# Performance work log

Hardware: AMD Instinct MI355X
Metric: run time of the kernel (lower is better)

Reference implementation:

```python
import jax, jax.numpy as jnp
import numpy as np

D_MODEL = 1024
NUM_HEADS = 16
HEAD_DIM = D_MODEL // NUM_HEADS
SEQ_LEN = 2048
BATCH = 2
THETA = 10000.0


def apply_rope(x, token_positions):
    # x: (..., seq, head_dim); token_positions: (seq,)
    d_k = x.shape[-1]
    inv_freq = 1.0 / (THETA ** (jnp.arange(0, d_k, 2, dtype=jnp.float32) / d_k))  # (d_k/2,)
    angle = token_positions.astype(jnp.float32)[:, None] * inv_freq[None, :]       # (seq, d_k/2)
    cos, sin = jnp.cos(angle), jnp.sin(angle)
    xr = x.reshape(*x.shape[:-1], d_k // 2, 2)
    a, b = xr[..., 0], xr[..., 1]  # real, imag parts of consecutive pairs
    # complex multiply (a + ib) * (cos + i sin)
    out_r = a * cos - b * sin
    out_i = a * sin + b * cos
    return jnp.stack([out_r, out_i], axis=-1).reshape(x.shape)


def setup_inputs() -> dict:
    key = jax.random.key(0)
    ks = jax.random.split(key, 5)
    std = np.sqrt(2.0 / (D_MODEL + D_MODEL))
    return {
        "x": jax.random.normal(ks[0], (BATCH, SEQ_LEN, D_MODEL), dtype=jnp.float32),
        "Wq": jax.random.normal(ks[1], (D_MODEL, D_MODEL), dtype=jnp.float32) * std,
        "Wk": jax.random.normal(ks[2], (D_MODEL, D_MODEL), dtype=jnp.float32) * std,
        "Wv": jax.random.normal(ks[3], (D_MODEL, D_MODEL), dtype=jnp.float32) * std,
        "Wo": jax.random.normal(ks[4], (D_MODEL, D_MODEL), dtype=jnp.float32) * std,
        "token_positions": jnp.arange(SEQ_LEN, dtype=jnp.int32),
    }


def reference(x, Wq, Wk, Wv, Wo, token_positions):
    B, L, D = x.shape
    H, Dh = NUM_HEADS, HEAD_DIM

    def proj(W):  # '... d_in, d_out d_in -> ... d_out' then split heads -> (B,H,L,Dh)
        y = jnp.einsum('bld,ed->ble', x, W)
        return y.reshape(B, L, H, Dh).transpose(0, 2, 1, 3)

    q = apply_rope(proj(Wq), token_positions)
    k = apply_rope(proj(Wk), token_positions)
    v = proj(Wv)

    scores = jnp.einsum('bhqd,bhkd->bhqk', q, k) / jnp.sqrt(jnp.float32(Dh))  # (B,H,L,L)
    causal = jnp.tril(jnp.ones((L, L), dtype=bool))
    scores = jnp.where(causal, scores, -jnp.inf)
    attn = jax.nn.softmax(scores, axis=-1)
    o = jnp.einsum('bhqk,bhkd->bhqd', attn, v)  # (B,H,L,Dh)
    o = o.transpose(0, 2, 1, 3).reshape(B, L, D)
    return jnp.einsum('bld,ed->ble', o, Wo)
```

## Files before the change

kernel.cpp:

```cpp
#include <hip/hip_runtime.h>

typedef __bf16 bf16;
typedef __attribute__((ext_vector_type(8))) __bf16 bf16x8;
typedef __attribute__((ext_vector_type(4))) __bf16 bf16x4;
typedef __attribute__((ext_vector_type(4))) float f32x4;

__device__ inline bf16 f2bf(float f) {
  unsigned u = __builtin_bit_cast(unsigned, f);
  u += 0x7fff + ((u >> 16) & 1);
  unsigned short h = (unsigned short)(u >> 16);
  return __builtin_bit_cast(bf16, h);
}

__device__ inline void gl_lds16(const bf16* g, bf16* l) {
  __builtin_amdgcn_global_load_lds(
      (const __attribute__((address_space(1))) void*)g,
      (__attribute__((address_space(3))) void*)l, 16, 0, 0);
}

__global__ __launch_bounds__(256) void cvt_kernel(
    const float* __restrict__ x, const float* __restrict__ wq,
    const float* __restrict__ wk, const float* __restrict__ wv,
    const float* __restrict__ wo, bf16* __restrict__ dst,
    const int* __restrict__ pos, float* __restrict__ tab) {
  if (blockIdx.x >= 8192) {
    int gid = (blockIdx.x - 8192) * 256 + threadIdx.x;
    int tok = gid >> 5, j = gid & 31;
    float freq = exp2f(-(float)(2 * j) * 0.20762051f);
    float angle = (float)pos[tok] * freq;
    float sn, cs;
    sincosf(angle, &sn, &cs);
    *(float2*)(tab + tok * 64 + j * 2) = make_float2(cs, sn);
    return;
  }
  int idx = (blockIdx.x * 256 + threadIdx.x) * 4;
  const float* src;
  if (idx < 4194304) {
    src = x + idx;
  } else {
    int j = idx - 4194304;
    int w = j >> 20;
    const float* sw = (w == 0) ? wq : (w == 1) ? wk : (w == 2) ? wv : wo;
    src = sw + (j & 1048575);
  }
  float4 f = *(const float4*)src;
  bf16x4 o = {f2bf(f.x), f2bf(f.y), f2bf(f.z), f2bf(f.w)};
  *(bf16x4*)(dst + idx) = o;
}

__global__ __launch_bounds__(256) void gemm_qkv_kernel(
    const bf16* __restrict__ xb, const bf16* __restrict__ wb,
    const float* __restrict__ tab,
    bf16* __restrict__ Qb, bf16* __restrict__ Kb, bf16* __restrict__ Vtb) {
  __shared__ __align__(16) bf16 smem[16384];
  int tid = threadIdx.x;
  int lane = tid & 63, w = tid >> 6;
  int l15 = lane & 15, quad = lane >> 4;
  int bid = blockIdx.x;
  int xcd = bid & 7, j = bid >> 3;
  int by = (xcd & 3) * 8 + (j & 7);
  int bx = (xcd >> 2) * 12 + (j >> 3);
  int mb = by * 128, nb = bx * 128;
  int mq = (w & 1) * 64, nq = (w >> 1) * 64;
  int rq = lane >> 2;
  int gsrc = (lane & 3) ^ (rq & 3) ^ (lane >> 4);
  const bf16* agp0 = xb + (size_t)(mb + w * 32 + rq) * 1024 + gsrc * 8;
  const bf16* agp1 = agp0 + 16 * 1024;
  const bf16* bgp0 = wb + (size_t)(nb + w * 32 + rq) * 1024 + gsrc * 8;
  const bf16* bgp1 = bgp0 + 16 * 1024;
  f32x4 acc[4][4];
#pragma unroll
  for (int i = 0; i < 4; ++i)
#pragma unroll
    for (int j2 = 0; j2 < 4; ++j2)
      for (int r = 0; r < 4; ++r) acc[i][j2][r] = 0.f;
  gl_lds16(agp0, smem + w * 1024);
  gl_lds16(agp1, smem + w * 1024 + 512);
  gl_lds16(bgp0, smem + 4096 + w * 1024);
  gl_lds16(bgp1, smem + 4096 + w * 1024 + 512);
  agp0 += 32; agp1 += 32; bgp0 += 32; bgp1 += 32;
  __syncthreads();
  int rg = quad ^ (l15 & 3) ^ (l15 >> 2);
  for (int kt = 0; kt < 32; ++kt) {
    bf16* Ab = smem + (kt & 1) * 8192;
    bf16* Bb = Ab + 4096;
    if (kt < 31) {
      bf16* An = smem + ((kt & 1) ^ 1) * 8192;
      bf16* Bn = An + 4096;
      gl_lds16(agp0, An + w * 1024);
      gl_lds16(agp1, An + w * 1024 + 512);
      gl_lds16(bgp0, Bn + w * 1024);
      gl_lds16(bgp1, Bn + w * 1024 + 512);
      agp0 += 32; agp1 += 32; bgp0 += 32; bgp1 += 32;
    }
    bf16x8 af[4], bfr[4];
#pragma unroll
    for (int mt = 0; mt < 4; ++mt)
      af[mt] = *(const bf16x8*)(Ab + (mq + mt * 16 + l15) * 32 + rg * 8);
#pragma unroll
    for (int nt = 0; nt < 4; ++nt)
      bfr[nt] = *(const bf16x8*)(Bb + (nq + nt * 16 + l15) * 32 + rg * 8);
#pragma unroll
    for (int mt = 0; mt < 4; ++mt)
#pragma unroll
      for (int nt = 0; nt < 4; ++nt)
        acc[mt][nt] = __builtin_amdgcn_mfma_f32_16x16x32_bf16(af[mt], bfr[nt], acc[mt][nt], 0, 0, 0);
    __syncthreads();
  }
  int b = mb >> 11;
  int mtok = mb & 2047;
  if (bx < 16) {
    bf16* dst = (bx < 8) ? Qb : Kb;
#pragma unroll
    for (int nt = 0; nt < 4; ++nt) {
      int e = nb + nq + nt * 16 + l15;
      int d = e & 63;
      int h = (e & 1023) >> 6;
      int tbase = d & ~1;
#pragma unroll
      for (int mt = 0; mt < 4; ++mt) {
#pragma unroll
        for (int r = 0; r < 4; ++r) {
          int ltok = mtok + mq + mt * 16 + quad * 4 + r;
          float val = acc[mt][nt][r];
          float p = __shfl_xor(val, 1);
          float2 cs2 = *(const float2*)(tab + ltok * 64 + tbase);
          float outv = (e & 1) ? (p * cs2.y + val * cs2.x) : (val * cs2.x - p * cs2.y);
          dst[(size_t)(((b << 4) + h) * 2048 + ltok) * 64 + d] = f2bf(outv);
        }
      }
    }
  } else {
    bf16* T = smem;
    for (int h2 = 0; h2 < 2; ++h2) {
      if ((w >> 1) == h2) {
#pragma unroll
        for (int nt = 0; nt < 4; ++nt)
#pragma unroll
          for (int mt = 0; mt < 4; ++mt) {
            bf16x4 tv = {f2bf(acc[mt][nt][0]), f2bf(acc[mt][nt][1]),
                         f2bf(acc[mt][nt][2]), f2bf(acc[mt][nt][3])};
            *(bf16x4*)&T[(nt * 16 + l15) * 136 + mq + mt * 16 + quad * 4] = tv;
          }
      }
      __syncthreads();
      int row = tid >> 2, cs = (tid & 3) * 32;
      int e = nb + h2 * 64 + row;
      int d = e & 63, hh = (e & 1023) >> 6;
      bf16* vdst = Vtb + ((size_t)((b << 4) + hh) * 64 + d) * 2048 + mtok + cs;
#pragma unroll
      for (int j3 = 0; j3 < 4; ++j3)
        *(bf16x8*)(vdst + j3 * 8) = *(const bf16x8*)&T[row * 136 + cs + j3 * 8];
      __syncthreads();
    }
  }
}

#define SCALE_L2E 0.18033688f
__global__ __launch_bounds__(256) void attn_kernel(
    const bf16* __restrict__ Qb, const bf16* __restrict__ Kb,
    const bf16* __restrict__ Vtb, bf16* __restrict__ Ob) {
  __shared__ __align__(16) bf16 Ks[64 * 64];
  __shared__ __align__(16) bf16 Vs[64 * 64];
  __shared__ __align__(16) bf16 pbuf[4][16 * 72];
  int tid = threadIdx.x;
  int lane = tid & 63, w = tid >> 6;
  int l15 = lane & 15, quad = lane >> 4;
  int bidx = blockIdx.x;
  int bh = bidx & 31;
  int qt = 31 - (bidx >> 5);
  int qbase = qt * 64;
  const bf16* Qp = Qb + (size_t)bh * 131072;
  const bf16* Kp = Kb + (size_t)bh * 131072;
  const bf16* Vp = Vtb + (size_t)bh * 131072;
  int r8 = lane >> 3;
  int gsw8 = (lane & 7) ^ r8;
  int g0 = quad ^ (l15 & 7);
  int g1 = (4 + quad) ^ (l15 & 7);
  bf16x8 qf[2];
#pragma unroll
  for (int c = 0; c < 2; ++c)
    qf[c] = *(const bf16x8*)(Qp + (size_t)(qbase + w * 16 + l15) * 64 + c * 32 + quad * 8);
  f32x4 oacc[4];
#pragma unroll
  for (int dt = 0; dt < 4; ++dt)
    for (int r = 0; r < 4; ++r) oacc[dt][r] = 0.f;
  float lpart = 0.f;
  int qmin_w = qbase + w * 16;
  int ntiles = qt + 1;

  {
    const bf16* ksrc = Kp + (size_t)(w * 16 + r8) * 64 + gsw8 * 8;
    bf16* kdst = &Ks[(w * 16) * 64];
    gl_lds16(ksrc, kdst);
    gl_lds16(ksrc + 8 * 64, kdst + 8 * 64);
    const bf16* vsrc = Vp + (size_t)(w * 16 + r8) * 2048 + gsw8 * 8;
    bf16* vdst = &Vs[(w * 16) * 64];
    gl_lds16(vsrc, vdst);
    gl_lds16(vsrc + 8 * 2048, vdst + 8 * 64);
  }
  __syncthreads();

  for (int t = 0; t < ntiles; ++t) {
    int kb = t * 64;
    bool pf = (t + 1 < ntiles);
    bf16x8 rk0, rk1, rv0, rv1;
    if (pf) {
      const bf16* ksrc = Kp + (size_t)(kb + 64 + w * 16 + r8) * 64 + gsw8 * 8;
      rk0 = *(const bf16x8*)ksrc;
      rk1 = *(const bf16x8*)(ksrc + 8 * 64);
      const bf16* vsrc = Vp + (size_t)(w * 16 + r8) * 2048 + kb + 64 + gsw8 * 8;
      rv0 = *(const bf16x8*)vsrc;
      rv1 = *(const bf16x8*)(vsrc + 8 * 2048);
    }
    {
      bf16x8 kf[4][2], vf[4][2];
#pragma unroll
      for (int kt = 0; kt < 4; ++kt) {
        kf[kt][0] = *(const bf16x8*)(&Ks[(kt * 16 + l15) * 64 + g0 * 8]);
        kf[kt][1] = *(const bf16x8*)(&Ks[(kt * 16 + l15) * 64 + g1 * 8]);
      }
#pragma unroll
      for (int dt = 0; dt < 4; ++dt) {
        vf[dt][0] = *(const bf16x8*)(&Vs[(dt * 16 + l15) * 64 + g0 * 8]);
        vf[dt][1] = *(const bf16x8*)(&Vs[(dt * 16 + l15) * 64 + g1 * 8]);
      }
      int q = qmin_w + l15;
      f32x4 s[4];
#pragma unroll
      for (int kt = 0; kt < 4; ++kt) {
        for (int r = 0; r < 4; ++r) s[kt][r] = 0.f;
        s[kt] = __builtin_amdgcn_mfma_f32_16x16x32_bf16(kf[kt][0], qf[0], s[kt], 0, 0, 0);
        s[kt] = __builtin_amdgcn_mfma_f32_16x16x32_bf16(kf[kt][1], qf[1], s[kt], 0, 0, 0);
      }
      float pe[16];
      if (kb + 63 > qmin_w) {
#pragma unroll
        for (int kt = 0; kt < 4; ++kt)
#pragma unroll
          for (int r = 0; r < 4; ++r) {
            int key = kb + kt * 16 + quad * 4 + r;
            pe[kt * 4 + r] = (key <= q) ? exp2f(s[kt][r] * SCALE_L2E) : 0.f;
          }
      } else {
#pragma unroll
        for (int kt = 0; kt < 4; ++kt)
#pragma unroll
          for (int r = 0; r < 4; ++r) pe[kt * 4 + r] = exp2f(s[kt][r] * SCALE_L2E);
      }
#pragma unroll
      for (int i = 0; i < 16; ++i) lpart += pe[i];
#pragma unroll
      for (int kt = 0; kt < 4; ++kt) {
        bf16x4 pw = {f2bf(pe[kt * 4]), f2bf(pe[kt * 4 + 1]), f2bf(pe[kt * 4 + 2]), f2bf(pe[kt * 4 + 3])};
        *(bf16x4*)&pbuf[w][l15 * 72 + kt * 16 + quad * 4] = pw;
      }
      bf16x8 pb0 = *(const bf16x8*)&pbuf[w][l15 * 72 + quad * 8];
      bf16x8 pb1 = *(const bf16x8*)&pbuf[w][l15 * 72 + 32 + quad * 8];
#pragma unroll
      for (int dt = 0; dt < 4; ++dt) {
        oacc[dt] = __builtin_amdgcn_mfma_f32_16x16x32_bf16(vf[dt][0], pb0, oacc[dt], 0, 0, 0);
        oacc[dt] = __builtin_amdgcn_mfma_f32_16x16x32_bf16(vf[dt][1], pb1, oacc[dt], 0, 0, 0);
      }
    }
    __syncthreads();
    if (pf) {
      bf16* kd = &Ks[(w * 16) * 64] + lane * 8;
      *(bf16x8*)kd = rk0;
      *(bf16x8*)(kd + 512) = rk1;
      bf16* vd = &Vs[(w * 16) * 64] + lane * 8;
      *(bf16x8*)vd = rv0;
      *(bf16x8*)(vd + 512) = rv1;
    }
    __syncthreads();
  }
  float lrun = lpart;
  lrun += __shfl_xor(lrun, 16);
  lrun += __shfl_xor(lrun, 32);
  int b0 = bh >> 4, h = bh & 15;
  float inv = 1.f / lrun;
  int q = qmin_w + l15;
  bf16* obase = Ob + ((size_t)(b0 * 2048 + q)) * 1024 + h * 64;
#pragma unroll
  for (int dt = 0; dt < 4; ++dt)
#pragma unroll
    for (int r = 0; r < 4; ++r)
      obase[dt * 16 + quad * 4 + r] = f2bf(oacc[dt][r] * inv);
}

__global__ __launch_bounds__(256) void gemm_out_kernel(
    const bf16* __restrict__ Ob, const bf16* __restrict__ wob,
    float* __restrict__ out) {
  __shared__ __align__(16) bf16 As[128 * 64];
  __shared__ __align__(16) bf16 Bs[64 * 64];
  int tid = threadIdx.x;
  int lane = tid & 63, w = tid >> 6;
  int l15 = lane & 15, quad = lane >> 4;
  int bid = blockIdx.x;
  int xcd = bid & 7, j = bid >> 3;
  int by = (xcd & 3) * 8 + (j & 7);
  int bx = (xcd >> 2) * 8 + (j >> 3);
  int mb = by * 128, nb = bx * 64;
  int mq = (w & 1) * 64, nq = (w >> 1) * 32;
  int gsw = (lane & 7) ^ ((lane >> 3) & 7);
  const bf16* agp = Ob + (size_t)(mb + w * 32 + (lane >> 3)) * 1024 + gsw * 8;
  const bf16* bgp = wob + (size_t)(nb + w * 16 + (lane >> 3)) * 1024 + gsw * 8;
  bf16* alp = As + (w * 32) * 64;
  bf16* blp = Bs + (w * 16) * 64;
  f32x4 acc[4][2];
#pragma unroll
  for (int i = 0; i < 4; ++i)
#pragma unroll
    for (int j2 = 0; j2 < 2; ++j2)
      for (int r = 0; r < 4; ++r) acc[i][j2][r] = 0.f;
  for (int kt = 0; kt < 16; ++kt) {
#pragma unroll
    for (int i = 0; i < 4; ++i)
      gl_lds16(agp + i * 8192, alp + i * 512);
#pragma unroll
    for (int i = 0; i < 2; ++i)
      gl_lds16(bgp + i * 8192, blp + i * 512);
    agp += 64; bgp += 64;
    __syncthreads();
#pragma unroll
    for (int c = 0; c < 2; ++c) {
      bf16x8 af[4], bfr[2];
      int rg = (c * 4 + quad);
#pragma unroll
      for (int mt = 0; mt < 4; ++mt)
        af[mt] = *(const bf16x8*)(As + (mq + mt * 16 + l15) * 64 + (rg ^ (l15 & 7)) * 8);
#pragma unroll
      for (int nt = 0; nt < 2; ++nt)
        bfr[nt] = *(const bf16x8*)(Bs + (nq + nt * 16 + l15) * 64 + (rg ^ (l15 & 7)) * 8);
#pragma unroll
      for (int mt = 0; mt < 4; ++mt)
#pragma unroll
        for (int nt = 0; nt < 2; ++nt)
          acc[mt][nt] = __builtin_amdgcn_mfma_f32_16x16x32_bf16(af[mt], bfr[nt], acc[mt][nt], 0, 0, 0);
    }
    __syncthreads();
  }
#pragma unroll
  for (int mt = 0; mt < 4; ++mt)
#pragma unroll
    for (int nt = 0; nt < 2; ++nt)
#pragma unroll
      for (int r = 0; r < 4; ++r)
        out[(size_t)(mb + mq + mt * 16 + quad * 4 + r) * 1024 + nb + nq + nt * 16 + l15] = acc[mt][nt][r];
}

extern "C" void kernel_launch(void* const* d_in, const int* in_sizes, int n_in,
                              void* d_out, int out_size, void* d_ws, size_t ws_size,
                              hipStream_t stream) {
  const float* x  = (const float*)d_in[0];
  const float* wq = (const float*)d_in[1];
  const float* wk = (const float*)d_in[2];
  const float* wv = (const float*)d_in[3];
  const float* wo = (const float*)d_in[4];
  const int* pos  = (const int*)d_in[5];
  float* out = (float*)d_out;
  bf16* wsb = (bf16*)d_ws;
  bf16* xb  = wsb;
  bf16* wb  = wsb + 4194304;
  bf16* Qb  = wsb + 8388608;
  bf16* Kb  = wsb + 12582912;
  bf16* Vtb = wsb + 16777216;
  bf16* Obf = wsb + 20971520;
  float* tab = (float*)Obf;
  hipLaunchKernelGGL(cvt_kernel, dim3(8448), dim3(256), 0, stream, x, wq, wk, wv, wo, wsb, pos, tab);
  hipLaunchKernelGGL(gemm_qkv_kernel, dim3(768), dim3(256), 0, stream, xb, wb, tab, Qb, Kb, Vtb);
  hipLaunchKernelGGL(attn_kernel, dim3(1024), dim3(256), 0, stream, Qb, Kb, Vtb, Obf);
  hipLaunchKernelGGL(gemm_out_kernel, dim3(512), dim3(256), 0, stream, Obf, wb + 3 * 1048576, out);
}
```

Measured before the change: 190.2 us.

## Load QKV A-operand directly to registers; double-buffer output GEMM LDS

In the QKV projection GEMM, the activation operand is no longer staged through LDS. Each wave loads its own A fragments straight from global memory into registers, ping-ponging between two register sets, and only the weight tile stays double-buffered in LDS, which shrinks shared memory. The output projection GEMM moves from a single-buffered 64-wide K tile with a sync before compute to a double-buffered 32-wide K tile that prefetches the next tile while computing. The aim is to cut LDS traffic and footprint and to hide global load latency. The cost is more register pressure and uncoalesced per-lane global reads for the A operand.

```diff
diff --git a/kernel.cpp b/kernel.cpp
--- a/kernel.cpp
+++ b/kernel.cpp
@@ -52,7 +52,7 @@
     const bf16* __restrict__ xb, const bf16* __restrict__ wb,
     const float* __restrict__ tab,
     bf16* __restrict__ Qb, bf16* __restrict__ Kb, bf16* __restrict__ Vtb) {
-  __shared__ __align__(16) bf16 smem[16384];
+  __shared__ __align__(16) bf16 smem[8704];
   int tid = threadIdx.x;
   int lane = tid & 63, w = tid >> 6;
   int l15 = lane & 15, quad = lane >> 4;
@@ -64,49 +64,58 @@
   int mq = (w & 1) * 64, nq = (w >> 1) * 64;
   int rq = lane >> 2;
   int gsrc = (lane & 3) ^ (rq & 3) ^ (lane >> 4);
-  const bf16* agp0 = xb + (size_t)(mb + w * 32 + rq) * 1024 + gsrc * 8;
-  const bf16* agp1 = agp0 + 16 * 1024;
   const bf16* bgp0 = wb + (size_t)(nb + w * 32 + rq) * 1024 + gsrc * 8;
   const bf16* bgp1 = bgp0 + 16 * 1024;
+  const bf16* agp = xb + (size_t)(mb + mq + l15) * 1024 + quad * 8;
   f32x4 acc[4][4];
 #pragma unroll
   for (int i = 0; i < 4; ++i)
 #pragma unroll
     for (int j2 = 0; j2 < 4; ++j2)
       for (int r = 0; r < 4; ++r) acc[i][j2][r] = 0.f;
-  gl_lds16(agp0, smem + w * 1024);
-  gl_lds16(agp1, smem + w * 1024 + 512);
-  gl_lds16(bgp0, smem + 4096 + w * 1024);
-  gl_lds16(bgp1, smem + 4096 + w * 1024 + 512);
-  agp0 += 32; agp1 += 32; bgp0 += 32; bgp1 += 32;
+  bf16x8 afA[4], afB[4];
+  gl_lds16(bgp0, smem + w * 1024);
+  gl_lds16(bgp1, smem + w * 1024 + 512);
+  bgp0 += 32; bgp1 += 32;
+#pragma unroll
+  for (int mt = 0; mt < 4; ++mt)
+    afA[mt] = *(const bf16x8*)(agp + mt * 16384);
   __syncthreads();
   int rg = quad ^ (l15 & 3) ^ (l15 >> 2);
-  for (int kt = 0; kt < 32; ++kt) {
-    bf16* Ab = smem + (kt & 1) * 8192;
-    bf16* Bb = Ab + 4096;
-    if (kt < 31) {
-      bf16* An = smem + ((kt & 1) ^ 1) * 8192;
-      bf16* Bn = An + 4096;
-      gl_lds16(agp0, An + w * 1024);
-      gl_lds16(agp1, An + w * 1024 + 512);
-      gl_lds16(bgp0, Bn + w * 1024);
-      gl_lds16(bgp1, Bn + w * 1024 + 512);
-      agp0 += 32; agp1 += 32; bgp0 += 32; bgp1 += 32;
-    }
-    bf16x8 af[4], bfr[4];
-#pragma unroll
-    for (int mt = 0; mt < 4; ++mt)
-      af[mt] = *(const bf16x8*)(Ab + (mq + mt * 16 + l15) * 32 + rg * 8);
-#pragma unroll
-    for (int nt = 0; nt < 4; ++nt)
-      bfr[nt] = *(const bf16x8*)(Bb + (nq + nt * 16 + l15) * 32 + rg * 8);
-#pragma unroll
-    for (int mt = 0; mt < 4; ++mt)
-#pragma unroll
-      for (int nt = 0; nt < 4; ++nt)
-        acc[mt][nt] = __builtin_amdgcn_mfma_f32_16x16x32_bf16(af[mt], bfr[nt], acc[mt][nt], 0, 0, 0);
-    __syncthreads();
-  }
+
+#define QKV_STEP(AFC, AFN)                                                    \
+  {                                                                           \
+    bf16* Bb = smem + (kt & 1) * 4096;                                        \
+    if (kt < 31) {       \
+      bf16* Bn = smem + ((kt & 1) ^ 1) * 4096;                                \
+      gl_lds16(bgp0, Bn + w * 1024);                                          \
+      gl_lds16(bgp1, Bn + w * 1024 + 512);                                    \
+      bgp0 += 32; bgp1 += 32;                                                 \
+      _Pragma("unroll") for (int mt = 0; mt < 4; ++mt)                        \
+          AFN[mt] = *(const bf16x8*)(agp + 32 + mt * 16384);                  \
+      agp += 32;                                                              \
+    }                                                                         \
+    bf16x8 bfr[4];                                                            \
+    _Pragma("unroll") for (int nt = 0; nt < 4; ++nt)                          \
+        bfr[nt] = *(const bf16x8*)(Bb + (nq + nt * 16 + l15) * 32 + rg * 8);  \
+    _Pragma("unroll") for (int mt = 0; mt < 4; ++mt)                          \
+        _Pragma("unroll") for (int nt = 0; nt < 4; ++nt)                      \
+            acc[mt][nt] = __builtin_amdgcn_mfma_f32_16x16x32_bf16(            \
+                AFC[mt], bfr[nt], acc[mt][nt], 0, 0, 0);                      \
+    __syncthreads();                                                          \
+  }
+
+  int kt = 0;
+  for (;;) {
+    QKV_STEP(afA, afB);
+    ++kt;
+    if (kt >= 32) break;
+    QKV_STEP(afB, afA);
+    ++kt;
+    if (kt >= 32) break;
+  }
+#undef QKV_STEP
+
   int b = mb >> 11;
   int mtok = mb & 2047;
   if (bx < 16) {
@@ -291,8 +300,7 @@
 __global__ __launch_bounds__(256) void gemm_out_kernel(
     const bf16* __restrict__ Ob, const bf16* __restrict__ wob,
     float* __restrict__ out) {
-  __shared__ __align__(16) bf16 As[128 * 64];
-  __shared__ __align__(16) bf16 Bs[64 * 64];
+  __shared__ __align__(16) bf16 smem[12288];
   int tid = threadIdx.x;
   int lane = tid & 63, w = tid >> 6;
   int l15 = lane & 15, quad = lane >> 4;
@@ -302,42 +310,45 @@
   int bx = (xcd >> 2) * 8 + (j >> 3);
   int mb = by * 128, nb = bx * 64;
   int mq = (w & 1) * 64, nq = (w >> 1) * 32;
-  int gsw = (lane & 7) ^ ((lane >> 3) & 7);
-  const bf16* agp = Ob + (size_t)(mb + w * 32 + (lane >> 3)) * 1024 + gsw * 8;
-  const bf16* bgp = wob + (size_t)(nb + w * 16 + (lane >> 3)) * 1024 + gsw * 8;
-  bf16* alp = As + (w * 32) * 64;
-  bf16* blp = Bs + (w * 16) * 64;
+  int rq = lane >> 2;
+  int gsrc = (lane & 3) ^ (rq & 3) ^ (lane >> 4);
+  const bf16* agp0 = Ob + (size_t)(mb + w * 32 + rq) * 1024 + gsrc * 8;
+  const bf16* agp1 = agp0 + 16 * 1024;
+  const bf16* bgp0 = wob + (size_t)(nb + w * 16 + rq) * 1024 + gsrc * 8;
   f32x4 acc[4][2];
 #pragma unroll
   for (int i = 0; i < 4; ++i)
 #pragma unroll
     for (int j2 = 0; j2 < 2; ++j2)
       for (int r = 0; r < 4; ++r) acc[i][j2][r] = 0.f;
-  for (int kt = 0; kt < 16; ++kt) {
-#pragma unroll
-    for (int i = 0; i < 4; ++i)
-      gl_lds16(agp + i * 8192, alp + i * 512);
-#pragma unroll
-    for (int i = 0; i < 2; ++i)
-      gl_lds16(bgp + i * 8192, blp + i * 512);
-    agp += 64; bgp += 64;
-    __syncthreads();
-#pragma unroll
-    for (int c = 0; c < 2; ++c) {
-      bf16x8 af[4], bfr[2];
-      int rg = (c * 4 + quad);
-#pragma unroll
-      for (int mt = 0; mt < 4; ++mt)
-        af[mt] = *(const bf16x8*)(As + (mq + mt * 16 + l15) * 64 + (rg ^ (l15 & 7)) * 8);
+  gl_lds16(agp0, smem + w * 1024);
+  gl_lds16(agp1, smem + w * 1024 + 512);
+  gl_lds16(bgp0, smem + 4096 + w * 512);
+  agp0 += 32; agp1 += 32; bgp0 += 32;
+  __syncthreads();
+  int rg = quad ^ (l15 & 3) ^ (l15 >> 2);
+  for (int kt = 0; kt < 32; ++kt) {
+    bf16* Ab = smem + (kt & 1) * 6144;
+    bf16* Bb = Ab + 4096;
+    if (kt < 31) {
+      bf16* An = smem + ((kt & 1) ^ 1) * 6144;
+      gl_lds16(agp0, An + w * 1024);
+      gl_lds16(agp1, An + w * 1024 + 512);
+      gl_lds16(bgp0, An + 4096 + w * 512);
+      agp0 += 32; agp1 += 32; bgp0 += 32;
+    }
+    bf16x8 af[4], bfr[2];
+#pragma unroll
+    for (int mt = 0; mt < 4; ++mt)
+      af[mt] = *(const bf16x8*)(Ab + (mq + mt * 16 + l15) * 32 + rg * 8);
+#pragma unroll
+    for (int nt = 0; nt < 2; ++nt)
+      bfr[nt] = *(const bf16x8*)(Bb + (nq + nt * 16 + l15) * 32 + rg * 8);
+#pragma unroll
+    for (int mt = 0; mt < 4; ++mt)
 #pragma unroll
       for (int nt = 0; nt < 2; ++nt)
-        bfr[nt] = *(const bf16x8*)(Bs + (nq + nt * 16 + l15) * 64 + (rg ^ (l15 & 7)) * 8);
-#pragma unroll
-      for (int mt = 0; mt < 4; ++mt)
-#pragma unroll
-        for (int nt = 0; nt < 2; ++nt)
-          acc[mt][nt] = __builtin_amdgcn_mfma_f32_16x16x32_bf16(af[mt], bfr[nt], acc[mt][nt], 0, 0, 0);
-    }
+        acc[mt][nt] = __builtin_amdgcn_mfma_f32_16x16x32_bf16(af[mt], bfr[nt], acc[mt][nt], 0, 0, 0);
     __syncthreads();
   }
 #pragma unroll
```

Result: slower. 231.4 us (+21.6%).
